# Optimization experiments

Hardware: AMD Instinct MI355X
Metric: run time of the kernel (lower is better)

Reference implementation:

```python
import jax, jax.numpy as jnp
import numpy as np

N, E = 4096, 131072
IN_DIM, HID, H = 128, 64, 8
D = HID * H          # 512 = d_model
DFF = HID * 4        # 256 (source uses hidden_dim*4, not d_model*4)
NEG_SLOPE = 0.2
LN_EPS = 1e-5


def setup_inputs() -> dict:
    key = jax.random.key(0)
    ks = jax.random.split(key, 24)
    r = lambda i, shp, s=0.05: (jax.random.normal(ks[i], shp, jnp.float32) * s)
    return {
        "x": jax.random.normal(ks[0], (N, IN_DIM), jnp.float32),
        "edge_index": jax.random.randint(ks[1], (2, E), 0, N, dtype=jnp.int32),
        "batch": jnp.zeros((N,), jnp.int32),
        "gat_lin_w": r(2, (D, IN_DIM)),
        "gat_att_src": r(3, (H, HID)),
        "gat_att_dst": r(4, (H, HID)),
        "gat_bias": jnp.zeros((D,), jnp.float32),
        "qkv_w": r(5, (2, 3 * D, D)),
        "qkv_b": jnp.zeros((2, 3 * D), jnp.float32),
        "out_w": r(6, (2, D, D)),
        "out_b": jnp.zeros((2, D), jnp.float32),
        "ln1_g": jnp.ones((2, D), jnp.float32),
        "ln1_b": jnp.zeros((2, D), jnp.float32),
        "ff1_w": r(7, (2, DFF, D)),
        "ff1_b": jnp.zeros((2, DFF), jnp.float32),
        "ff2_w": r(8, (2, D, DFF)),
        "ff2_b": jnp.zeros((2, D), jnp.float32),
        "ln2_g": jnp.ones((2, D), jnp.float32),
        "ln2_b": jnp.zeros((2, D), jnp.float32),
    }


def _layer_norm(x, g, b):
    mu = jnp.mean(x, -1, keepdims=True)
    var = jnp.mean(jnp.square(x - mu), -1, keepdims=True)
    return (x - mu) * jax.lax.rsqrt(var + LN_EPS) * g + b


def _gat(x, edge_index, lin_w, att_src, att_dst, bias):
    # PyG GATConv: linear -> per-edge leaky_relu attention -> softmax over dst -> scatter-add
    h = (x @ lin_w.T).reshape(N, H, HID)                 # [N,H,C]
    loops = jnp.arange(N, dtype=edge_index.dtype)        # add_self_loops=True (PyG default)
    src = jnp.concatenate([edge_index[0], loops])
    dst = jnp.concatenate([edge_index[1], loops])
    a_src = jnp.einsum('nhc,hc->nh', h, att_src)         # [N,H]
    a_dst = jnp.einsum('nhc,hc->nh', h, att_dst)
    e = jax.nn.leaky_relu(a_src[src] + a_dst[dst], NEG_SLOPE)   # [E+N,H]
    emax = jax.ops.segment_max(e, dst, num_segments=N)          # self-loops => no empty segment
    p = jnp.exp(e - emax[dst])
    denom = jax.ops.segment_sum(p, dst, num_segments=N)
    alpha = p / (denom[dst] + 1e-16)                             # [E+N,H]
    msg = alpha[..., None] * h[src]                              # [E+N,H,C]
    out = jax.ops.segment_sum(msg, dst, num_segments=N)         # [N,H,C]
    return out.reshape(N, D) + bias


def _mha(x, w_qkv, b_qkv, w_o, b_o):
    qkv = x @ w_qkv.T + b_qkv                            # [N,3D]
    q, k, v = jnp.split(qkv, 3, axis=-1)
    q = q.reshape(N, H, HID).transpose(1, 0, 2)          # [H,N,c]
    k = k.reshape(N, H, HID).transpose(1, 0, 2)
    v = v.reshape(N, H, HID).transpose(1, 0, 2)
    scores = jnp.einsum('hnc,hmc->hnm', q, k) / jnp.sqrt(jnp.float32(HID))
    attn = jax.nn.softmax(scores, axis=-1)
    o = jnp.einsum('hnm,hmc->hnc', attn, v).transpose(1, 0, 2).reshape(N, D)
    return o @ w_o.T + b_o


def reference(x, edge_index, batch, gat_lin_w, gat_att_src, gat_att_dst, gat_bias,
              qkv_w, qkv_b, out_w, out_b, ln1_g, ln1_b,
              ff1_w, ff1_b, ff2_w, ff2_b, ln2_g, ln2_b):
    h = _gat(x, edge_index, gat_lin_w, gat_att_src, gat_att_dst, gat_bias)
    # TransformerEncoder, 2 post-norm layers, relu FFN, dropout=0; seq_len=N, batch=1
    for i in range(2):
        a = _mha(h, qkv_w[i], qkv_b[i], out_w[i], out_b[i])
        h = _layer_norm(h + a, ln1_g[i], ln1_b[i])
        f = jax.nn.relu(h @ ff1_w[i].T + ff1_b[i]) @ ff2_w[i].T + ff2_b[i]
        h = _layer_norm(h + f, ln2_g[i], ln2_b[i])
    return h
```

## Files before the change

kernel.cpp:

```cpp
#include <hip/hip_runtime.h>
#include <math.h>

#define NN    4096
#define EE    131072
#define ENE   (EE + NN)
#define IND   128
#define HH    8
#define HIDC  64
#define DD    512
#define D3    1536
#define DFF2  256

typedef __attribute__((ext_vector_type(8))) short short8;
typedef __attribute__((ext_vector_type(4))) float f32x4;
typedef __attribute__((ext_vector_type(2))) unsigned int uint2v;

__device__ __forceinline__ float lrelu02(float x) { return x >= 0.f ? x : 0.2f * x; }

__device__ __forceinline__ unsigned short f2bf(float x) {
    unsigned int u = __float_as_uint(x);
    u += 0x7fffu + ((u >> 16) & 1u);
    return (unsigned short)(u >> 16);
}
__device__ __forceinline__ float bf2f(unsigned short u) {
    return __uint_as_float((unsigned int)u << 16);
}
__device__ __forceinline__ unsigned int cvt_pk_bf16(float lo, float hi) {
    unsigned int r;
    asm("v_cvt_pk_bf16_f32 %0, %1, %2" : "=v"(r) : "v"(lo), "v"(hi));
    return r;
}
__device__ __forceinline__ float max3f(float a, float b, float c) {
    float r;
    asm("v_max3_f32 %0, %1, %2, %3" : "=v"(r) : "v"(a), "v"(b), "v"(c));
    return r;
}

struct CvtJobs {
    const float* src[6];
    unsigned short* dst[6];
    int n[6];
};

__global__ __launch_bounds__(256) void cvt_many(CvtJobs jb, int total)
{
    int i = (blockIdx.x * 256 + threadIdx.x) * 4;
    if (i >= total) return;
    int s = 0;
    while (i >= jb.n[s]) { i -= jb.n[s]; ++s; }
    float4 v = *(const float4*)(jb.src[s] + i);
    unsigned int lo = (unsigned int)f2bf(v.x) | ((unsigned int)f2bf(v.y) << 16);
    unsigned int hi = (unsigned int)f2bf(v.z) | ((unsigned int)f2bf(v.w) << 16);
    uint2v pk; pk.x = lo; pk.y = hi;
    *(uint2v*)(jb.dst[s] + i) = pk;
}

__global__ __launch_bounds__(256) void gemm_bf16(const unsigned short* __restrict__ A,
                                                 const unsigned short* __restrict__ W,
                                                 const float* __restrict__ bias,
                                                 void* __restrict__ C,
                                                 int M, int K, int N, int flags)
{
    __shared__ __align__(16) unsigned short As[128 * 64];
    __shared__ __align__(16) unsigned short Bs[128 * 64];

    const int t = threadIdx.x, lane = t & 63, w = t >> 6;
    const int wr = w >> 1, wc = w & 1;
    const int bm = blockIdx.y * 128, bn = blockIdx.x * 128;
    const int q = lane & 15, g = lane >> 4;

    f32x4 acc[4][4];
#pragma unroll
    for (int m = 0; m < 4; ++m)
#pragma unroll
        for (int n = 0; n < 4; ++n) acc[m][n] = (f32x4){0.f, 0.f, 0.f, 0.f};

    const int srow = t >> 1, sh = t & 1;
    const unsigned short* Ag = A + (size_t)(bm + srow) * K + sh * 32;
    const unsigned short* Wg = W + (size_t)(bn + srow) * K + sh * 32;
    int wofs[4];
#pragma unroll
    for (int i = 0; i < 4; ++i)
        wofs[i] = srow * 128 + ((((sh * 4 + i) * 16) ^ ((srow & 7) << 4)));

    for (int k0 = 0; k0 < K; k0 += 64) {
        short8 av[4], bv[4];
#pragma unroll
        for (int i = 0; i < 4; ++i) {
            av[i] = *(const short8*)(Ag + k0 + i * 8);
            bv[i] = *(const short8*)(Wg + k0 + i * 8);
        }
        __syncthreads();
#pragma unroll
        for (int i = 0; i < 4; ++i) {
            *(short8*)((char*)As + wofs[i]) = av[i];
            *(short8*)((char*)Bs + wofs[i]) = bv[i];
        }
        __syncthreads();

        short8 af[2][4], bfr[2][4];
#pragma unroll
        for (int m = 0; m < 4; ++m) {
            const int row = wr * 64 + m * 16 + q;
#pragma unroll
            for (int kk = 0; kk < 2; ++kk)
                af[kk][m] = *(const short8*)((const char*)As +
                    row * 128 + ((((kk * 4 + g) * 16) ^ ((row & 7) << 4))));
        }
#pragma unroll
        for (int n = 0; n < 4; ++n) {
            const int row = wc * 64 + n * 16 + q;
#pragma unroll
            for (int kk = 0; kk < 2; ++kk)
                bfr[kk][n] = *(const short8*)((const char*)Bs +
                    row * 128 + ((((kk * 4 + g) * 16) ^ ((row & 7) << 4))));
        }
#pragma unroll
        for (int kk = 0; kk < 2; ++kk)
#pragma unroll
            for (int m = 0; m < 4; ++m)
#pragma unroll
                for (int n = 0; n < 4; ++n)
                    acc[m][n] = __builtin_amdgcn_mfma_f32_16x16x32_bf16(
                        bfr[kk][n], af[kk][m], acc[m][n], 0, 0, 0);
    }

    const int obf = flags & 1, orelu = flags & 2, oqs = flags & 4;
#pragma unroll
    for (int m = 0; m < 4; ++m) {
        const int row = bm + wr * 64 + m * 16 + q;
#pragma unroll
        for (int n = 0; n < 4; ++n) {
            const int col0 = bn + wc * 64 + n * 16 + g * 4;
            f32x4 v = acc[m][n];
            if (bias) {
                float4 bv4 = *(const float4*)(bias + col0);
                v[0] += bv4.x; v[1] += bv4.y; v[2] += bv4.z; v[3] += bv4.w;
            }
            if (oqs && col0 < DD) {
                const float qs = 0.18033688f;
                v[0] *= qs; v[1] *= qs; v[2] *= qs; v[3] *= qs;
            }
            if (orelu) {
                v[0] = fmaxf(v[0], 0.f); v[1] = fmaxf(v[1], 0.f);
                v[2] = fmaxf(v[2], 0.f); v[3] = fmaxf(v[3], 0.f);
            }
            if (obf) {
                uint2v pk;
                pk.x = (unsigned int)f2bf(v[0]) | ((unsigned int)f2bf(v[1]) << 16);
                pk.y = (unsigned int)f2bf(v[2]) | ((unsigned int)f2bf(v[3]) << 16);
                *(uint2v*)((unsigned short*)C + (size_t)row * N + col0) = pk;
            } else {
                float4 o; o.x = v[0]; o.y = v[1]; o.z = v[2]; o.w = v[3];
                *(float4*)((float*)C + (size_t)row * N + col0) = o;
            }
        }
    }
}

__global__ __launch_bounds__(256) void gemm64(const unsigned short* __restrict__ A,
                                              const unsigned short* __restrict__ W,
                                              const float* __restrict__ bias,
                                              void* __restrict__ C,
                                              int M, int K, int N, int flags)
{
    __shared__ __align__(16) unsigned short As[64 * 64];
    __shared__ __align__(16) unsigned short Bs[64 * 64];

    const int t = threadIdx.x, lane = t & 63, w = t >> 6;
    const int wr = w >> 1, wc = w & 1;
    const int bm = blockIdx.y * 64, bn = blockIdx.x * 64;
    const int q = lane & 15, g = lane >> 4;

    f32x4 acc[2][2];
#pragma unroll
    for (int m = 0; m < 2; ++m)
#pragma unroll
        for (int n = 0; n < 2; ++n) acc[m][n] = (f32x4){0.f, 0.f, 0.f, 0.f};

    const int srow = t >> 2, sh = t & 3;
    const unsigned short* Ag = A + (size_t)(bm + srow) * K + sh * 16;
    const unsigned short* Wg = W + (size_t)(bn + srow) * K + sh * 16;
    int wofs[2];
#pragma unroll
    for (int i = 0; i < 2; ++i)
        wofs[i] = srow * 128 + ((((sh * 2 + i) * 16) ^ ((srow & 7) << 4)));

    for (int k0 = 0; k0 < K; k0 += 64) {
        short8 av[2], bv[2];
#pragma unroll
        for (int i = 0; i < 2; ++i) {
            av[i] = *(const short8*)(Ag + k0 + i * 8);
            bv[i] = *(const short8*)(Wg + k0 + i * 8);
        }
        __syncthreads();
#pragma unroll
        for (int i = 0; i < 2; ++i) {
            *(short8*)((char*)As + wofs[i]) = av[i];
            *(short8*)((char*)Bs + wofs[i]) = bv[i];
        }
        __syncthreads();

        short8 af[2][2], bfr[2][2];
#pragma unroll
        for (int m = 0; m < 2; ++m) {
            const int row = wr * 32 + m * 16 + q;
#pragma unroll
            for (int kk = 0; kk < 2; ++kk)
                af[kk][m] = *(const short8*)((const char*)As +
                    row * 128 + ((((kk * 4 + g) * 16) ^ ((row & 7) << 4))));
        }
#pragma unroll
        for (int n = 0; n < 2; ++n) {
            const int row = wc * 32 + n * 16 + q;
#pragma unroll
            for (int kk = 0; kk < 2; ++kk)
                bfr[kk][n] = *(const short8*)((const char*)Bs +
                    row * 128 + ((((kk * 4 + g) * 16) ^ ((row & 7) << 4))));
        }
#pragma unroll
        for (int kk = 0; kk < 2; ++kk)
#pragma unroll
            for (int m = 0; m < 2; ++m)
#pragma unroll
                for (int n = 0; n < 2; ++n)
                    acc[m][n] = __builtin_amdgcn_mfma_f32_16x16x32_bf16(
                        bfr[kk][n], af[kk][m], acc[m][n], 0, 0, 0);
    }

    const int obf = flags & 1, orelu = flags & 2;
#pragma unroll
    for (int m = 0; m < 2; ++m) {
        const int row = bm + wr * 32 + m * 16 + q;
#pragma unroll
        for (int n = 0; n < 2; ++n) {
            const int col0 = bn + wc * 32 + n * 16 + g * 4;
            f32x4 v = acc[m][n];
            if (bias) {
                float4 bv4 = *(const float4*)(bias + col0);
                v[0] += bv4.x; v[1] += bv4.y; v[2] += bv4.z; v[3] += bv4.w;
            }
            if (orelu) {
                v[0] = fmaxf(v[0], 0.f); v[1] = fmaxf(v[1], 0.f);
                v[2] = fmaxf(v[2], 0.f); v[3] = fmaxf(v[3], 0.f);
            }
            if (obf) {
                uint2v pk;
                pk.x = (unsigned int)f2bf(v[0]) | ((unsigned int)f2bf(v[1]) << 16);
                pk.y = (unsigned int)f2bf(v[2]) | ((unsigned int)f2bf(v[3]) << 16);
                *(uint2v*)((unsigned short*)C + (size_t)row * N + col0) = pk;
            } else {
                float4 o; o.x = v[0]; o.y = v[1]; o.z = v[2]; o.w = v[3];
                *(float4*)((float*)C + (size_t)row * N + col0) = o;
            }
        }
    }
}

__global__ void att_proj(const unsigned short* __restrict__ hlin,
                         const float* __restrict__ att_s,
                         const float* __restrict__ att_d,
                         float* __restrict__ a_src, float* __restrict__ a_dst)
{
    int idx = blockIdx.x * 256 + threadIdx.x;
    if (idx >= NN * HH) return;
    int n = idx >> 3, h = idx & 7;
    const unsigned short* hp = hlin + (size_t)n * DD + h * HIDC;
    const float* as = att_s + h * HIDC;
    const float* ad = att_d + h * HIDC;
    float s1 = 0.f, s2 = 0.f;
#pragma unroll 8
    for (int c = 0; c < HIDC; ++c) {
        float hv = bf2f(hp[c]);
        s1 += hv * as[c]; s2 += hv * ad[c];
    }
    a_src[idx] = s1;
    a_dst[idx] = s2;
}

__global__ void hist_kernel(const int* __restrict__ ei, int* __restrict__ counts)
{
    int i = blockIdx.x * 256 + threadIdx.x;
    if (i >= ENE) return;
    int dst = (i < EE) ? ei[EE + i] : (i - EE);
    atomicAdd(&counts[dst], 1);
}

__global__ __launch_bounds__(1024) void scan_kernel(const int* __restrict__ counts,
                                                    int* __restrict__ offsets)
{
    __shared__ int sums[1024];
    int t = threadIdx.x;
    int v0 = counts[t*4+0], v1 = counts[t*4+1], v2 = counts[t*4+2], v3 = counts[t*4+3];
    sums[t] = v0 + v1 + v2 + v3;
    __syncthreads();
    for (int off = 1; off < 1024; off <<= 1) {
        int x = (t >= off) ? sums[t - off] : 0;
        __syncthreads();
        sums[t] += x;
        __syncthreads();
    }
    int pre = (t > 0) ? sums[t-1] : 0;
    offsets[t*4+0] = pre;
    offsets[t*4+1] = pre + v0;
    offsets[t*4+2] = pre + v0 + v1;
    offsets[t*4+3] = pre + v0 + v1 + v2;
    if (t == 1023) offsets[4096] = sums[1023];
}

__global__ void scatter_kernel(const int* __restrict__ ei, const int* __restrict__ offs,
                               int* __restrict__ cursor, int* __restrict__ src_sorted)
{
    int i = blockIdx.x * 256 + threadIdx.x;
    if (i >= ENE) return;
    int s, d;
    if (i < EE) { s = ei[i]; d = ei[EE + i]; } else { s = d = i - EE; }
    int pos = atomicAdd(&cursor[d], 1);
    src_sorted[offs[d] + pos] = s;
}

__global__ __launch_bounds__(256) void gat_node(const unsigned short* __restrict__ hlin,
                                                const float* __restrict__ a_src,
                                                const float* __restrict__ a_dst,
                                                const int* __restrict__ offs,
                                                const int* __restrict__ src_sorted,
                                                const float* __restrict__ bias,
                                                float* __restrict__ out,
                                                unsigned short* __restrict__ outb)
{
    __shared__ float adst[8];
    __shared__ float emax[8];
    __shared__ float denom[8];
    __shared__ float red[256];
    __shared__ float p_lds[16][8];
    __shared__ int   srcs[16];

    const int n = blockIdx.x, t = threadIdx.x;
    if (t < 8) { adst[t] = a_dst[n * 8 + t]; denom[t] = 0.f; }
    const int off0 = offs[n];
    const int deg  = offs[n+1] - off0;
    __syncthreads();

    const int h = t & 7, slot = t >> 3;
    float mx = -3.0e38f;
    for (int j = slot; j < deg; j += 32) {
        int s = src_sorted[off0 + j];
        mx = fmaxf(mx, a_src[s * 8 + h] + adst[h]);
    }
    red[t] = mx;
    __syncthreads();
    for (int half = 128; half >= 8; half >>= 1) {
        if (t < half) red[t] = fmaxf(red[t], red[t + half]);
        __syncthreads();
    }
    if (t < 8) emax[t] = lrelu02(red[t]);
    __syncthreads();

    float acc0 = 0.f, acc1 = 0.f;
    const int h0 = t >> 6, h1 = (t + 256) >> 6;
    for (int base = 0; base < deg; base += 16) {
        int cnt = min(16, deg - base);
        if (t < cnt * 8) {
            int j = base + (t >> 3);
            int s = src_sorted[off0 + j];
            if ((t & 7) == 0) srcs[t >> 3] = s;
            float x = a_src[s * 8 + (t & 7)] + adst[t & 7];
            float p = __expf(lrelu02(x) - emax[t & 7]);
            p_lds[t >> 3][t & 7] = p;
            atomicAdd(&denom[t & 7], p);
        }
        __syncthreads();
        for (int jj = 0; jj < cnt; ++jj) {
            int s = srcs[jj];
            const unsigned short* hp = hlin + (size_t)s * DD;
            acc0 += p_lds[jj][h0] * bf2f(hp[t]);
            acc1 += p_lds[jj][h1] * bf2f(hp[256 + t]);
        }
        __syncthreads();
    }
    float o0 = acc0 / (denom[h0] + 1e-16f) + bias[t];
    float o1 = acc1 / (denom[h1] + 1e-16f) + bias[256 + t];
    out[(size_t)n * DD + t]        = o0;
    out[(size_t)n * DD + 256 + t]  = o1;
    outb[(size_t)n * DD + t]       = f2bf(o0);
    outb[(size_t)n * DD + 256 + t] = f2bf(o1);
}

#define KVB 128
#define NTT (NN / KVB)

__global__ __launch_bounds__(256) void attn_mfma(const unsigned short* __restrict__ qkv,
                                                 unsigned short* __restrict__ aob)
{
    __shared__ __align__(16) unsigned short Ks0[KVB * 64];
    __shared__ __align__(16) unsigned short Vt0[80 * KVB];
    __shared__ __align__(16) unsigned short Ks1[KVB * 64];
    __shared__ __align__(16) unsigned short Vt1[80 * KVB];

    const int t = threadIdx.x;
    const int w = t >> 6, lane = t & 63;
    const int q15 = lane & 15, g = lane >> 4;

    const int fid = blockIdx.x;
    const int h = fid & 7, qb = fid >> 3;
    const int qbase = qb * 64 + w * 16;

    const unsigned short* qrow = qkv + (size_t)(qbase + q15) * D3 + h * HIDC;
    const short8 qf0 = *(const short8*)(qrow + g * 8);
    const short8 qf1 = *(const short8*)(qrow + 32 + g * 8);

    f32x4 O[4];
#pragma unroll
    for (int db = 0; db < 4; ++db) O[db] = (f32x4){0.f, 0.f, 0.f, 0.f};
    f32x4 O5 = (f32x4){0.f, 0.f, 0.f, 0.f};
    float m_run = -3.0e38f;

    int koff[8][2];
#pragma unroll
    for (int kvb = 0; kvb < 8; ++kvb) {
        const int kr = kvb * 16 + q15;
        koff[kvb][0] = (kr * 64 + g * 8) ^ ((kr & 7) << 3);
        koff[kvb][1] = (kr * 64 + 32 + g * 8) ^ ((kr & 7) << 3);
    }
    int voff[4][4];
#pragma unroll
    for (int db = 0; db < 4; ++db) {
        const int vr = db * 16 + q15;
#pragma unroll
        for (int ks = 0; ks < 4; ++ks)
            voff[db][ks] = (vr * KVB + ks * 32 + g * 8) ^ ((vr & 7) << 3);
    }
    int voffE[4];
#pragma unroll
    for (int ks = 0; ks < 4; ++ks) {
        const int rv = 64 + q15;
        voffE[ks] = (rv * KVB + ks * 32 + g * 8) ^ ((rv & 7) << 3);
    }
    const int kr_s = t >> 1, sh = t & 1;
    const int kq = t & 31, dg = t >> 5;
    const int slot4 = (kq >> 3) * 32 + (kq & 3) * 8 + ((kq >> 2) & 1) * 4;
    int kwoff[4];
#pragma unroll
    for (int i = 0; i < 4; ++i)
        kwoff[i] = (kr_s * 64 + (sh * 4 + i) * 8) ^ ((kr_s & 7) << 3);
    int vwoff[8];
#pragma unroll
    for (int i = 0; i < 8; ++i) {
        const int d = dg * 8 + i;
        vwoff[i] = (d * KVB + slot4) ^ ((d & 7) << 3);
    }
    const unsigned short* Kg = qkv + (size_t)kr_s * D3 + DD + h * HIDC + sh * 32;
    const unsigned short* Vg = qkv + (size_t)(4 * kq) * D3 + 2 * DD + h * HIDC + dg * 8;

    short8 kreg[4], vreg[4];

    auto LOAD_KV = [&](int kb) {
        const size_t off = (size_t)kb * KVB * D3;
#pragma unroll
        for (int i = 0; i < 4; ++i) kreg[i] = *(const short8*)(Kg + off + i * 8);
#pragma unroll
        for (int jj = 0; jj < 4; ++jj) vreg[jj] = *(const short8*)(Vg + off + (size_t)jj * D3);
    };
    auto WRITE_KV = [&](unsigned short* KD, unsigned short* VD) {
#pragma unroll
        for (int i = 0; i < 4; ++i)
            *(short8*)&KD[kwoff[i]] = kreg[i];
        const unsigned int* w0 = (const unsigned int*)&vreg[0];
        const unsigned int* w1 = (const unsigned int*)&vreg[1];
        const unsigned int* w2 = (const unsigned int*)&vreg[2];
        const unsigned int* w3 = (const unsigned int*)&vreg[3];
#pragma unroll
        for (int i = 0; i < 8; ++i) {
            const unsigned int sel = (i & 1) ? 0x07060302u : 0x05040100u;
            uint2v pk;
            pk.x = __builtin_amdgcn_perm(w1[i >> 1], w0[i >> 1], sel);
            pk.y = __builtin_amdgcn_perm(w3[i >> 1], w2[i >> 1], sel);
            *(uint2v*)&VD[vwoff[i]] = pk;
        }
    };

    auto TILE = [&](int kb, const unsigned short* BK, const unsigned short* BV,
                    unsigned short* NK, unsigned short* NV) {
        const int kbn = kb + 1;
        if (kbn < NTT) LOAD_KV(kbn);

        f32x4 st[8];
        __builtin_amdgcn_s_setprio(1);
#pragma unroll
        for (int kvb = 0; kvb < 8; ++kvb) {
            const short8 kf0 = *(const short8*)&BK[koff[kvb][0]];
            const short8 kf1 = *(const short8*)&BK[koff[kvb][1]];
            f32x4 acc = (f32x4){0.f, 0.f, 0.f, 0.f};
            acc = __builtin_amdgcn_mfma_f32_16x16x32_bf16(kf0, qf0, acc, 0, 0, 0);
            acc = __builtin_amdgcn_mfma_f32_16x16x32_bf16(kf1, qf1, acc, 0, 0, 0);
            st[kvb] = acc;
        }
        __builtin_amdgcn_s_setprio(0);

        float pm0 = max3f(st[0][0], st[0][1], st[0][2]);
        float pm1 = max3f(st[0][3], st[1][0], st[1][1]);
        float pm2 = max3f(st[1][2], st[1][3], st[2][0]);
        float pm3 = max3f(st[2][1], st[2][2], st[2][3]);
        float pm4 = max3f(st[3][0], st[3][1], st[3][2]);
        float pm5 = max3f(st[3][3], st[4][0], st[4][1]);
        float pm6 = max3f(st[4][2], st[4][3], st[5][0]);
        float pm7 = max3f(st[5][1], st[5][2], st[5][3]);
        float pm8 = max3f(st[6][0], st[6][1], st[6][2]);
        float pm9 = max3f(st[6][3], st[7][0], st[7][1]);
        float pmA = max3f(st[7][2], st[7][3], pm0);
        float q0 = max3f(pm1, pm2, pm3);
        float q1 = max3f(pm4, pm5, pm6);
        float q2 = max3f(pm7, pm8, pm9);
        float pmax = max3f(q0, q1, q2);
        pmax = fmaxf(pmax, pmA);
        pmax = fmaxf(pmax, __shfl_xor(pmax, 16, 64));
        pmax = fmaxf(pmax, __shfl_xor(pmax, 32, 64));
        if (!__all(pmax <= m_run + 11.f)) {
            const float mnew = fmaxf(m_run, pmax);
            const float f = exp2f(m_run - mnew);
#pragma unroll
            for (int db = 0; db < 4; ++db) O[db] *= f;
            O5 *= f;
            m_run = mnew;
        }

        short8 pf[4];
#pragma unroll
        for (int ks = 0; ks < 4; ++ks) {
            float e0 = exp2f(st[2*ks  ][0] - m_run), e1 = exp2f(st[2*ks  ][1] - m_run);
            float e2 = exp2f(st[2*ks  ][2] - m_run), e3 = exp2f(st[2*ks  ][3] - m_run);
            float e4 = exp2f(st[2*ks+1][0] - m_run), e5 = exp2f(st[2*ks+1][1] - m_run);
            float e6 = exp2f(st[2*ks+1][2] - m_run), e7 = exp2f(st[2*ks+1][3] - m_run);
            union { unsigned int u[4]; short8 s8; } pu;
            pu.u[0] = cvt_pk_bf16(e0, e1);
            pu.u[1] = cvt_pk_bf16(e2, e3);
            pu.u[2] = cvt_pk_bf16(e4, e5);
            pu.u[3] = cvt_pk_bf16(e6, e7);
            pf[ks] = pu.s8;
        }

        __builtin_amdgcn_s_setprio(1);
#pragma unroll
        for (int db = 0; db < 4; ++db) {
#pragma unroll
            for (int ks = 0; ks < 4; ++ks) {
                const short8 vf = *(const short8*)&BV[voff[db][ks]];
                O[db] = __builtin_amdgcn_mfma_f32_16x16x32_bf16(vf, pf[ks], O[db], 0, 0, 0);
            }
        }
#pragma unroll
        for (int ks = 0; ks < 4; ++ks) {
            const short8 vfE = *(const short8*)&BV[voffE[ks]];
            O5 = __builtin_amdgcn_mfma_f32_16x16x32_bf16(vfE, pf[ks], O5, 0, 0, 0);
        }
        __builtin_amdgcn_s_setprio(0);

        if (kbn < NTT) {
            WRITE_KV(NK, NV);
            __syncthreads();
        }
    };

    {
        const int d = 64 + (t >> 4), c = (t & 15) * 8;
        short8 iv;
#pragma unroll
        for (int i = 0; i < 8; ++i)
            iv[i] = (short)((d == 64) ? 0x3F80 : 0);
        const int ofs = (d * KVB + c) ^ ((d & 7) << 3);
        *(short8*)&Vt0[ofs] = iv;
        *(short8*)&Vt1[ofs] = iv;
    }
    LOAD_KV(0);
    WRITE_KV(Ks0, Vt0);
    __syncthreads();

    for (int kb = 0; kb < NTT; kb += 2) {
        TILE(kb,     Ks0, Vt0, Ks1, Vt1);
        TILE(kb + 1, Ks1, Vt1, Ks0, Vt0);
    }

    const float lsum = __shfl(O5[0], q15, 64);
    const float linv = 1.f / lsum;
#pragma unroll
    for (int db = 0; db < 4; ++db) {
        uint2v pk;
        pk.x = (unsigned int)f2bf(O[db][0] * linv) | ((unsigned int)f2bf(O[db][1] * linv) << 16);
        pk.y = (unsigned int)f2bf(O[db][2] * linv) | ((unsigned int)f2bf(O[db][3] * linv) << 16);
        *(uint2v*)&aob[(size_t)(qbase + q15) * DD + h * HIDC + db * 16 + g * 4] = pk;
    }
}

__global__ __launch_bounds__(256) void ln_fused(const float* __restrict__ hin,
                                                const float* __restrict__ dlt,
                                                const float* __restrict__ g,
                                                const float* __restrict__ b,
                                                float* __restrict__ out,
                                                unsigned short* __restrict__ outb)
{
    __shared__ float red[256];
    const int r = blockIdx.x, t = threadIdx.x;
    const size_t base = (size_t)r * DD;
    float v0 = hin[base + t] + dlt[base + t];
    float v1 = hin[base + 256 + t] + dlt[base + 256 + t];
    red[t] = v0 + v1;
    __syncthreads();
    for (int off = 128; off > 0; off >>= 1) { if (t < off) red[t] += red[t + off]; __syncthreads(); }
    float mu = red[0] * (1.f / 512.f);
    __syncthreads();
    float d0 = v0 - mu, d1 = v1 - mu;
    red[t] = d0 * d0 + d1 * d1;
    __syncthreads();
    for (int off = 128; off > 0; off >>= 1) { if (t < off) red[t] += red[t + off]; __syncthreads(); }
    float rs = rsqrtf(red[0] * (1.f / 512.f) + 1e-5f);
    float o0 = d0 * rs * g[t] + b[t];
    float o1 = d1 * rs * g[256 + t] + b[256 + t];
    out[base + t]       = o0;
    out[base + 256 + t] = o1;
    if (outb) {
        outb[base + t]       = f2bf(o0);
        outb[base + 256 + t] = f2bf(o1);
    }
}

extern "C" void kernel_launch(void* const* d_in, const int* in_sizes, int n_in,
                              void* d_out, int out_size, void* d_ws, size_t ws_size,
                              hipStream_t stream)
{
    (void)in_sizes; (void)n_in; (void)out_size; (void)ws_size;

    const float* x        = (const float*)d_in[0];
    const int*   ei       = (const int*)  d_in[1];
    const float* lin_w    = (const float*)d_in[3];
    const float* att_src  = (const float*)d_in[4];
    const float* att_dst  = (const float*)d_in[5];
    const float* gat_bias = (const float*)d_in[6];
    const float* qkv_w    = (const float*)d_in[7];
    const float* qkv_b    = (const float*)d_in[8];
    const float* out_w    = (const float*)d_in[9];
    const float* out_b    = (const float*)d_in[10];
    const float* ln1_g    = (const float*)d_in[11];
    const float* ln1_b    = (const float*)d_in[12];
    const float* ff1_w    = (const float*)d_in[13];
    const float* ff1_b    = (const float*)d_in[14];
    const float* ff2_w    = (const float*)d_in[15];
    const float* ff2_b    = (const float*)d_in[16];
    const float* ln2_g    = (const float*)d_in[17];
    const float* ln2_b    = (const float*)d_in[18];

    char* wsb = (char*)d_ws;
    size_t o = 0;
    auto alloc = [&](size_t bytes) { char* p = wsb + o; o += (bytes + 255) & ~(size_t)255; return p; };

    unsigned short* hlin_bf = (unsigned short*)alloc((size_t)NN * DD * 2);
    unsigned short* hbf     = (unsigned short*)alloc((size_t)NN * DD * 2);
    unsigned short* qkv16   = (unsigned short*)alloc((size_t)NN * D3 * 2);
    unsigned short* aob     = (unsigned short*)alloc((size_t)NN * DD * 2);
    unsigned short* ff1obf  = (unsigned short*)alloc((size_t)NN * DFF2 * 2);
    float* hcur  = (float*)alloc((size_t)NN * DD * 4);
    float* tmp1  = (float*)alloc((size_t)NN * DD * 4);
    float* a_src = (float*)alloc((size_t)NN * HH * 4);
    float* a_dst = (float*)alloc((size_t)NN * HH * 4);
    int* counts     = (int*)alloc(NN * 4);
    int* cursor     = (int*)alloc(NN * 4);
    int* offsets    = (int*)alloc((NN + 1) * 4);
    int* src_sorted = (int*)alloc(ENE * 4);
    unsigned short* xbf    = (unsigned short*)alloc((size_t)NN * IND * 2);
    unsigned short* linwbf = (unsigned short*)alloc((size_t)DD * IND * 2);
    unsigned short* qkvwbf = (unsigned short*)alloc((size_t)2 * D3 * DD * 2);
    unsigned short* outwbf = (unsigned short*)alloc((size_t)2 * DD * DD * 2);
    unsigned short* ff1wbf = (unsigned short*)alloc((size_t)2 * DFF2 * DD * 2);
    unsigned short* ff2wbf = (unsigned short*)alloc((size_t)2 * DD * DFF2 * 2);

    CvtJobs jb;
    jb.src[0] = x;      jb.dst[0] = xbf;    jb.n[0] = NN * IND;
    jb.src[1] = lin_w;  jb.dst[1] = linwbf; jb.n[1] = DD * IND;
    jb.src[2] = qkv_w;  jb.dst[2] = qkvwbf; jb.n[2] = 2 * D3 * DD;
    jb.src[3] = out_w;  jb.dst[3] = outwbf; jb.n[3] = 2 * DD * DD;
    jb.src[4] = ff1_w;  jb.dst[4] = ff1wbf; jb.n[4] = 2 * DFF2 * DD;
    jb.src[5] = ff2_w;  jb.dst[5] = ff2wbf; jb.n[5] = 2 * DD * DFF2;
    int cvt_total = jb.n[0]+jb.n[1]+jb.n[2]+jb.n[3]+jb.n[4]+jb.n[5];
    cvt_many<<<(cvt_total/4 + 255)/256, 256, 0, stream>>>(jb, cvt_total);

    hipMemsetAsync(counts, 0, 2 * NN * sizeof(int), stream);
    gemm64<<<dim3(DD/64, NN/64), 256, 0, stream>>>(xbf, linwbf, nullptr, hlin_bf,
                                                   NN, IND, DD, 1);
    att_proj<<<(NN*HH + 255)/256, 256, 0, stream>>>(hlin_bf, att_src, att_dst, a_src, a_dst);
    hist_kernel<<<(ENE + 255)/256, 256, 0, stream>>>(ei, counts);
    scan_kernel<<<1, 1024, 0, stream>>>(counts, offsets);
    scatter_kernel<<<(ENE + 255)/256, 256, 0, stream>>>(ei, offsets, cursor, src_sorted);
    gat_node<<<NN, 256, 0, stream>>>(hlin_bf, a_src, a_dst, offsets, src_sorted, gat_bias,
                                     hcur, hbf);

    for (int i = 0; i < 2; ++i) {
        gemm_bf16<<<dim3(D3/128, NN/128), 256, 0, stream>>>(hbf, qkvwbf + (size_t)i*D3*DD,
                                                            qkv_b + (size_t)i*D3, qkv16,
                                                            NN, DD, D3, 1 | 4);
        attn_mfma<<<dim3(NN/64 * HH), 256, 0, stream>>>(qkv16, aob);
        gemm64<<<dim3(DD/64, NN/64), 256, 0, stream>>>(aob, outwbf + (size_t)i*DD*DD,
                                                       out_b + (size_t)i*DD, tmp1,
                                                       NN, DD, DD, 0);
        ln_fused<<<NN, 256, 0, stream>>>(hcur, tmp1, ln1_g + (size_t)i*DD, ln1_b + (size_t)i*DD,
                                         hcur, hbf);
        gemm64<<<dim3(DFF2/64, NN/64), 256, 0, stream>>>(hbf, ff1wbf + (size_t)i*DFF2*DD,
                                                         ff1_b + (size_t)i*DFF2, ff1obf,
                                                         NN, DD, DFF2, 1 | 2);
        gemm64<<<dim3(DD/64, NN/64), 256, 0, stream>>>(ff1obf, ff2wbf + (size_t)i*DD*DFF2,
                                                       ff2_b + (size_t)i*DD, tmp1,
                                                       NN, DFF2, DD, 0);
        float* outp = (i == 1) ? (float*)d_out : hcur;
        unsigned short* outbp = (i == 1) ? nullptr : hbf;
        ln_fused<<<NN, 256, 0, stream>>>(hcur, tmp1, ln2_g + (size_t)i*DD, ln2_b + (size_t)i*DD,
                                         outp, outbp);
    }
}
```

Baseline: 332.8 us.

## Process two query tiles per wave in attention, store residual deltas as bf16

```diff
diff --git a/kernel.cpp b/kernel.cpp
--- a/kernel.cpp
+++ b/kernel.cpp
@@ -389,8 +389,8 @@
 #define KVB 128
 #define NTT (NN / KVB)
 
-__global__ __launch_bounds__(256) void attn_mfma(const unsigned short* __restrict__ qkv,
-                                                 unsigned short* __restrict__ aob)
+__global__ __launch_bounds__(128, 1) void attn_mfma(const unsigned short* __restrict__ qkv,
+                                                    unsigned short* __restrict__ aob)
 {
     __shared__ __align__(16) unsigned short Ks0[KVB * 64];
     __shared__ __align__(16) unsigned short Vt0[80 * KVB];
@@ -403,17 +403,24 @@
 
     const int fid = blockIdx.x;
     const int h = fid & 7, qb = fid >> 3;
-    const int qbase = qb * 64 + w * 16;
-
-    const unsigned short* qrow = qkv + (size_t)(qbase + q15) * D3 + h * HIDC;
-    const short8 qf0 = *(const short8*)(qrow + g * 8);
-    const short8 qf1 = *(const short8*)(qrow + 32 + g * 8);
-
-    f32x4 O[4];
-#pragma unroll
-    for (int db = 0; db < 4; ++db) O[db] = (f32x4){0.f, 0.f, 0.f, 0.f};
-    f32x4 O5 = (f32x4){0.f, 0.f, 0.f, 0.f};
-    float m_run = -3.0e38f;
+    const int qbase = qb * 64 + w * 32;
+
+    const unsigned short* qrow0 = qkv + (size_t)(qbase + q15) * D3 + h * HIDC;
+    const unsigned short* qrow1 = qrow0 + (size_t)16 * D3;
+    const short8 qf00 = *(const short8*)(qrow0 + g * 8);
+    const short8 qf01 = *(const short8*)(qrow0 + 32 + g * 8);
+    const short8 qf10 = *(const short8*)(qrow1 + g * 8);
+    const short8 qf11 = *(const short8*)(qrow1 + 32 + g * 8);
+
+    f32x4 O0[4], O1[4];
+#pragma unroll
+    for (int db = 0; db < 4; ++db) {
+        O0[db] = (f32x4){0.f, 0.f, 0.f, 0.f};
+        O1[db] = (f32x4){0.f, 0.f, 0.f, 0.f};
+    }
+    f32x4 O5a = (f32x4){0.f, 0.f, 0.f, 0.f};
+    f32x4 O5b = (f32x4){0.f, 0.f, 0.f, 0.f};
+    float m0 = -3.0e38f, m1 = -3.0e38f;
 
     int koff[8][2];
 #pragma unroll
@@ -436,46 +443,53 @@
         const int rv = 64 + q15;
         voffE[ks] = (rv * KVB + ks * 32 + g * 8) ^ ((rv & 7) << 3);
     }
-    const int kr_s = t >> 1, sh = t & 1;
+
+    const int krow = t;
     const int kq = t & 31, dg = t >> 5;
     const int slot4 = (kq >> 3) * 32 + (kq & 3) * 8 + ((kq >> 2) & 1) * 4;
-    int kwoff[4];
-#pragma unroll
-    for (int i = 0; i < 4; ++i)
-        kwoff[i] = (kr_s * 64 + (sh * 4 + i) * 8) ^ ((kr_s & 7) << 3);
-    int vwoff[8];
-#pragma unroll
-    for (int i = 0; i < 8; ++i) {
-        const int d = dg * 8 + i;
+    int kwoff[8];
+#pragma unroll
+    for (int i = 0; i < 8; ++i)
+        kwoff[i] = (krow * 64 + i * 8) ^ ((krow & 7) << 3);
+    int vwoff[16];
+#pragma unroll
+    for (int i = 0; i < 16; ++i) {
+        const int d = dg * 16 + i;
         vwoff[i] = (d * KVB + slot4) ^ ((d & 7) << 3);
     }
-    const unsigned short* Kg = qkv + (size_t)kr_s * D3 + DD + h * HIDC + sh * 32;
-    const unsigned short* Vg = qkv + (size_t)(4 * kq) * D3 + 2 * DD + h * HIDC + dg * 8;
-
-    short8 kreg[4], vreg[4];
+    const unsigned short* Kg = qkv + (size_t)krow * D3 + DD + h * HIDC;
+    const unsigned short* Vg = qkv + (size_t)(4 * kq) * D3 + 2 * DD + h * HIDC + dg * 16;
+
+    short8 kreg[8], vreg[4][2];
 
     auto LOAD_KV = [&](int kb) {
         const size_t off = (size_t)kb * KVB * D3;
 #pragma unroll
-        for (int i = 0; i < 4; ++i) kreg[i] = *(const short8*)(Kg + off + i * 8);
-#pragma unroll
-        for (int jj = 0; jj < 4; ++jj) vreg[jj] = *(const short8*)(Vg + off + (size_t)jj * D3);
+        for (int i = 0; i < 8; ++i) kreg[i] = *(const short8*)(Kg + off + i * 8);
+#pragma unroll
+        for (int j = 0; j < 4; ++j)
+#pragma unroll
+            for (int c = 0; c < 2; ++c)
+                vreg[j][c] = *(const short8*)(Vg + off + (size_t)j * D3 + c * 8);
     };
     auto WRITE_KV = [&](unsigned short* KD, unsigned short* VD) {
 #pragma unroll
-        for (int i = 0; i < 4; ++i)
+        for (int i = 0; i < 8; ++i)
             *(short8*)&KD[kwoff[i]] = kreg[i];
-        const unsigned int* w0 = (const unsigned int*)&vreg[0];
-        const unsigned int* w1 = (const unsigned int*)&vreg[1];
-        const unsigned int* w2 = (const unsigned int*)&vreg[2];
-        const unsigned int* w3 = (const unsigned int*)&vreg[3];
-#pragma unroll
-        for (int i = 0; i < 8; ++i) {
-            const unsigned int sel = (i & 1) ? 0x07060302u : 0x05040100u;
-            uint2v pk;
-            pk.x = __builtin_amdgcn_perm(w1[i >> 1], w0[i >> 1], sel);
-            pk.y = __builtin_amdgcn_perm(w3[i >> 1], w2[i >> 1], sel);
-            *(uint2v*)&VD[vwoff[i]] = pk;
+#pragma unroll
+        for (int c = 0; c < 2; ++c) {
+            const unsigned int* w0 = (const unsigned int*)&vreg[0][c];
+            const unsigned int* w1 = (const unsigned int*)&vreg[1][c];
+            const unsigned int* w2 = (const unsigned int*)&vreg[2][c];
+            const unsigned int* w3 = (const unsigned int*)&vreg[3][c];
+#pragma unroll
+            for (int i = 0; i < 8; ++i) {
+                const unsigned int sel = (i & 1) ? 0x07060302u : 0x05040100u;
+                uint2v pk;
+                pk.x = __builtin_amdgcn_perm(w1[i >> 1], w0[i >> 1], sel);
+                pk.y = __builtin_amdgcn_perm(w3[i >> 1], w2[i >> 1], sel);
+                *(uint2v*)&VD[vwoff[c * 8 + i]] = pk;
+            }
         }
     };
 
@@ -484,59 +498,71 @@
         const int kbn = kb + 1;
         if (kbn < NTT) LOAD_KV(kbn);
 
-        f32x4 st[8];
+        f32x4 st0[8], st1[8];
         __builtin_amdgcn_s_setprio(1);
 #pragma unroll
         for (int kvb = 0; kvb < 8; ++kvb) {
             const short8 kf0 = *(const short8*)&BK[koff[kvb][0]];
             const short8 kf1 = *(const short8*)&BK[koff[kvb][1]];
-            f32x4 acc = (f32x4){0.f, 0.f, 0.f, 0.f};
-            acc = __builtin_amdgcn_mfma_f32_16x16x32_bf16(kf0, qf0, acc, 0, 0, 0);
-            acc = __builtin_amdgcn_mfma_f32_16x16x32_bf16(kf1, qf1, acc, 0, 0, 0);
-            st[kvb] = acc;
+            f32x4 a0 = (f32x4){0.f, 0.f, 0.f, 0.f};
+            f32x4 a1 = (f32x4){0.f, 0.f, 0.f, 0.f};
+            a0 = __builtin_amdgcn_mfma_f32_16x16x32_bf16(kf0, qf00, a0, 0, 0, 0);
+            a1 = __builtin_amdgcn_mfma_f32_16x16x32_bf16(kf0, qf10, a1, 0, 0, 0);
+            a0 = __builtin_amdgcn_mfma_f32_16x16x32_bf16(kf1, qf01, a0, 0, 0, 0);
+            a1 = __builtin_amdgcn_mfma_f32_16x16x32_bf16(kf1, qf11, a1, 0, 0, 0);
+            st0[kvb] = a0;
+            st1[kvb] = a1;
         }
         __builtin_amdgcn_s_setprio(0);
 
-        float pm0 = max3f(st[0][0], st[0][1], st[0][2]);
-        float pm1 = max3f(st[0][3], st[1][0], st[1][1]);
-        float pm2 = max3f(st[1][2], st[1][3], st[2][0]);
-        float pm3 = max3f(st[2][1], st[2][2], st[2][3]);
-        float pm4 = max3f(st[3][0], st[3][1], st[3][2]);
-        float pm5 = max3f(st[3][3], st[4][0], st[4][1]);
-        float pm6 = max3f(st[4][2], st[4][3], st[5][0]);
-        float pm7 = max3f(st[5][1], st[5][2], st[5][3]);
-        float pm8 = max3f(st[6][0], st[6][1], st[6][2]);
-        float pm9 = max3f(st[6][3], st[7][0], st[7][1]);
-        float pmA = max3f(st[7][2], st[7][3], pm0);
-        float q0 = max3f(pm1, pm2, pm3);
-        float q1 = max3f(pm4, pm5, pm6);
-        float q2 = max3f(pm7, pm8, pm9);
-        float pmax = max3f(q0, q1, q2);
-        pmax = fmaxf(pmax, pmA);
-        pmax = fmaxf(pmax, __shfl_xor(pmax, 16, 64));
-        pmax = fmaxf(pmax, __shfl_xor(pmax, 32, 64));
-        if (!__all(pmax <= m_run + 11.f)) {
-            const float mnew = fmaxf(m_run, pmax);
-            const float f = exp2f(m_run - mnew);
-#pragma unroll
-            for (int db = 0; db < 4; ++db) O[db] *= f;
-            O5 *= f;
-            m_run = mnew;
-        }
-
-        short8 pf[4];
-#pragma unroll
-        for (int ks = 0; ks < 4; ++ks) {
-            float e0 = exp2f(st[2*ks  ][0] - m_run), e1 = exp2f(st[2*ks  ][1] - m_run);
-            float e2 = exp2f(st[2*ks  ][2] - m_run), e3 = exp2f(st[2*ks  ][3] - m_run);
-            float e4 = exp2f(st[2*ks+1][0] - m_run), e5 = exp2f(st[2*ks+1][1] - m_run);
-            float e6 = exp2f(st[2*ks+1][2] - m_run), e7 = exp2f(st[2*ks+1][3] - m_run);
-            union { unsigned int u[4]; short8 s8; } pu;
-            pu.u[0] = cvt_pk_bf16(e0, e1);
-            pu.u[1] = cvt_pk_bf16(e2, e3);
-            pu.u[2] = cvt_pk_bf16(e4, e5);
-            pu.u[3] = cvt_pk_bf16(e6, e7);
-            pf[ks] = pu.s8;
+        short8 pf0[4], pf1[4];
+#pragma unroll
+        for (int qg = 0; qg < 2; ++qg) {
+            f32x4* st = qg ? st1 : st0;
+            f32x4* O  = qg ? O1  : O0;
+            f32x4& O5 = qg ? O5b : O5a;
+            float& m_run = qg ? m1 : m0;
+            short8* pf = qg ? pf1 : pf0;
+
+            float pm0 = max3f(st[0][0], st[0][1], st[0][2]);
+            float pm1 = max3f(st[0][3], st[1][0], st[1][1]);
+            float pm2 = max3f(st[1][2], st[1][3], st[2][0]);
+            float pm3 = max3f(st[2][1], st[2][2], st[2][3]);
+            float pm4 = max3f(st[3][0], st[3][1], st[3][2]);
+            float pm5 = max3f(st[3][3], st[4][0], st[4][1]);
+            float pm6 = max3f(st[4][2], st[4][3], st[5][0]);
+            float pm7 = max3f(st[5][1], st[5][2], st[5][3]);
+            float pm8 = max3f(st[6][0], st[6][1], st[6][2]);
+            float pm9 = max3f(st[6][3], st[7][0], st[7][1]);
+            float pmA = max3f(st[7][2], st[7][3], pm0);
+            float r0 = max3f(pm1, pm2, pm3);
+            float r1 = max3f(pm4, pm5, pm6);
+            float r2 = max3f(pm7, pm8, pm9);
+            float pmax = max3f(r0, r1, r2);
+            pmax = fmaxf(pmax, pmA);
+            pmax = fmaxf(pmax, __shfl_xor(pmax, 16, 64));
+            pmax = fmaxf(pmax, __shfl_xor(pmax, 32, 64));
+            if (!__all(pmax <= m_run + 11.f)) {
+                const float mnew = fmaxf(m_run, pmax);
+                const float f = exp2f(m_run - mnew);
+#pragma unroll
+                for (int db = 0; db < 4; ++db) O[db] *= f;
+                O5 *= f;
+                m_run = mnew;
+            }
+#pragma unroll
+            for (int ks = 0; ks < 4; ++ks) {
+                float e0 = exp2f(st[2*ks  ][0] - m_run), e1 = exp2f(st[2*ks  ][1] - m_run);
+                float e2 = exp2f(st[2*ks  ][2] - m_run), e3 = exp2f(st[2*ks  ][3] - m_run);
+                float e4 = exp2f(st[2*ks+1][0] - m_run), e5 = exp2f(st[2*ks+1][1] - m_run);
+                float e6 = exp2f(st[2*ks+1][2] - m_run), e7 = exp2f(st[2*ks+1][3] - m_run);
+                union { unsigned int u[4]; short8 s8; } pu;
+                pu.u[0] = cvt_pk_bf16(e0, e1);
+                pu.u[1] = cvt_pk_bf16(e2, e3);
+                pu.u[2] = cvt_pk_bf16(e4, e5);
+                pu.u[3] = cvt_pk_bf16(e6, e7);
+                pf[ks] = pu.s8;
+            }
         }
 
         __builtin_amdgcn_s_setprio(1);
@@ -545,13 +571,15 @@
 #pragma unroll
             for (int ks = 0; ks < 4; ++ks) {
                 const short8 vf = *(const short8*)&BV[voff[db][ks]];
-                O[db] = __builtin_amdgcn_mfma_f32_16x16x32_bf16(vf, pf[ks], O[db], 0, 0, 0);
+                O0[db] = __builtin_amdgcn_mfma_f32_16x16x32_bf16(vf, pf0[ks], O0[db], 0, 0, 0);
+                O1[db] = __builtin_amdgcn_mfma_f32_16x16x32_bf16(vf, pf1[ks], O1[db], 0, 0, 0);
             }
         }
 #pragma unroll
         for (int ks = 0; ks < 4; ++ks) {
             const short8 vfE = *(const short8*)&BV[voffE[ks]];
-            O5 = __builtin_amdgcn_mfma_f32_16x16x32_bf16(vfE, pf[ks], O5, 0, 0, 0);
+            O5a = __builtin_amdgcn_mfma_f32_16x16x32_bf16(vfE, pf0[ks], O5a, 0, 0, 0);
+            O5b = __builtin_amdgcn_mfma_f32_16x16x32_bf16(vfE, pf1[ks], O5b, 0, 0, 0);
         }
         __builtin_amdgcn_s_setprio(0);
 
@@ -562,14 +590,15 @@
     };
 
     {
-        const int d = 64 + (t >> 4), c = (t & 15) * 8;
+        const int d = 64 + (t >> 3), c = (t & 7) * 16;
         short8 iv;
 #pragma unroll
         for (int i = 0; i < 8; ++i)
             iv[i] = (short)((d == 64) ? 0x3F80 : 0);
-        const int ofs = (d * KVB + c) ^ ((d & 7) << 3);
-        *(short8*)&Vt0[ofs] = iv;
-        *(short8*)&Vt1[ofs] = iv;
+        const int ofs0 = (d * KVB + c) ^ ((d & 7) << 3);
+        const int ofs1 = (d * KVB + c + 8) ^ ((d & 7) << 3);
+        *(short8*)&Vt0[ofs0] = iv; *(short8*)&Vt0[ofs1] = iv;
+        *(short8*)&Vt1[ofs0] = iv; *(short8*)&Vt1[ofs1] = iv;
     }
     LOAD_KV(0);
     WRITE_KV(Ks0, Vt0);
@@ -580,19 +609,25 @@
         TILE(kb + 1, Ks1, Vt1, Ks0, Vt0);
     }
 
-    const float lsum = __shfl(O5[0], q15, 64);
-    const float linv = 1.f / lsum;
-#pragma unroll
-    for (int db = 0; db < 4; ++db) {
-        uint2v pk;
-        pk.x = (unsigned int)f2bf(O[db][0] * linv) | ((unsigned int)f2bf(O[db][1] * linv) << 16);
-        pk.y = (unsigned int)f2bf(O[db][2] * linv) | ((unsigned int)f2bf(O[db][3] * linv) << 16);
-        *(uint2v*)&aob[(size_t)(qbase + q15) * DD + h * HIDC + db * 16 + g * 4] = pk;
+#pragma unroll
+    for (int qg = 0; qg < 2; ++qg) {
+        const f32x4* O  = qg ? O1  : O0;
+        const f32x4& O5 = qg ? O5b : O5a;
+        const float lsum = __shfl(O5[0], q15, 64);
+        const float linv = 1.f / lsum;
+        const size_t row = (size_t)(qbase + qg * 16 + q15);
+#pragma unroll
+        for (int db = 0; db < 4; ++db) {
+            uint2v pk;
+            pk.x = (unsigned int)f2bf(O[db][0] * linv) | ((unsigned int)f2bf(O[db][1] * linv) << 16);
+            pk.y = (unsigned int)f2bf(O[db][2] * linv) | ((unsigned int)f2bf(O[db][3] * linv) << 16);
+            *(uint2v*)&aob[row * DD + h * HIDC + db * 16 + g * 4] = pk;
+        }
     }
 }
 
 __global__ __launch_bounds__(256) void ln_fused(const float* __restrict__ hin,
-                                                const float* __restrict__ dlt,
+                                                const unsigned short* __restrict__ dlt,
                                                 const float* __restrict__ g,
                                                 const float* __restrict__ b,
                                                 float* __restrict__ out,
@@ -601,8 +636,10 @@
     __shared__ float red[256];
     const int r = blockIdx.x, t = threadIdx.x;
     const size_t base = (size_t)r * DD;
-    float v0 = hin[base + t] + dlt[base + t];
-    float v1 = hin[base + 256 + t] + dlt[base + 256 + t];
+    float2 hv = *(const float2*)(hin + base + 2 * t);
+    unsigned int dv = *(const unsigned int*)(dlt + base + 2 * t);
+    float v0 = hv.x + bf2f((unsigned short)(dv & 0xffffu));
+    float v1 = hv.y + bf2f((unsigned short)(dv >> 16));
     red[t] = v0 + v1;
     __syncthreads();
     for (int off = 128; off > 0; off >>= 1) { if (t < off) red[t] += red[t + off]; __syncthreads(); }
@@ -613,13 +650,15 @@
     __syncthreads();
     for (int off = 128; off > 0; off >>= 1) { if (t < off) red[t] += red[t + off]; __syncthreads(); }
     float rs = rsqrtf(red[0] * (1.f / 512.f) + 1e-5f);
-    float o0 = d0 * rs * g[t] + b[t];
-    float o1 = d1 * rs * g[256 + t] + b[256 + t];
-    out[base + t]       = o0;
-    out[base + 256 + t] = o1;
+    float2 gv = *(const float2*)(g + 2 * t);
+    float2 bv = *(const float2*)(b + 2 * t);
+    float o0 = d0 * rs * gv.x + bv.x;
+    float o1 = d1 * rs * gv.y + bv.y;
+    float2 ov; ov.x = o0; ov.y = o1;
+    *(float2*)(out + base + 2 * t) = ov;
     if (outb) {
-        outb[base + t]       = f2bf(o0);
-        outb[base + 256 + t] = f2bf(o1);
+        unsigned int pk = (unsigned int)f2bf(o0) | ((unsigned int)f2bf(o1) << 16);
+        *(unsigned int*)(outb + base + 2 * t) = pk;
     }
 }
 
@@ -657,8 +696,8 @@
     unsigned short* qkv16   = (unsigned short*)alloc((size_t)NN * D3 * 2);
     unsigned short* aob     = (unsigned short*)alloc((size_t)NN * DD * 2);
     unsigned short* ff1obf  = (unsigned short*)alloc((size_t)NN * DFF2 * 2);
+    unsigned short* dltbf   = (unsigned short*)alloc((size_t)NN * DD * 2);
     float* hcur  = (float*)alloc((size_t)NN * DD * 4);
-    float* tmp1  = (float*)alloc((size_t)NN * DD * 4);
     float* a_src = (float*)alloc((size_t)NN * HH * 4);
     float* a_dst = (float*)alloc((size_t)NN * HH * 4);
     int* counts     = (int*)alloc(NN * 4);
@@ -696,21 +735,21 @@
         gemm_bf16<<<dim3(D3/128, NN/128), 256, 0, stream>>>(hbf, qkvwbf + (size_t)i*D3*DD,
                                                             qkv_b + (size_t)i*D3, qkv16,
                                                             NN, DD, D3, 1 | 4);
-        attn_mfma<<<dim3(NN/64 * HH), 256, 0, stream>>>(qkv16, aob);
+        attn_mfma<<<dim3(NN/64 * HH), 128, 0, stream>>>(qkv16, aob);
         gemm64<<<dim3(DD/64, NN/64), 256, 0, stream>>>(aob, outwbf + (size_t)i*DD*DD,
-                                                       out_b + (size_t)i*DD, tmp1,
-                                                       NN, DD, DD, 0);
-        ln_fused<<<NN, 256, 0, stream>>>(hcur, tmp1, ln1_g + (size_t)i*DD, ln1_b + (size_t)i*DD,
+                                                       out_b + (size_t)i*DD, dltbf,
+                                                       NN, DD, DD, 1);
+        ln_fused<<<NN, 256, 0, stream>>>(hcur, dltbf, ln1_g + (size_t)i*DD, ln1_b + (size_t)i*DD,
                                          hcur, hbf);
         gemm64<<<dim3(DFF2/64, NN/64), 256, 0, stream>>>(hbf, ff1wbf + (size_t)i*DFF2*DD,
                                                          ff1_b + (size_t)i*DFF2, ff1obf,
                                                          NN, DD, DFF2, 1 | 2);
         gemm64<<<dim3(DD/64, NN/64), 256, 0, stream>>>(ff1obf, ff2wbf + (size_t)i*DD*DFF2,
-                                                       ff2_b + (size_t)i*DD, tmp1,
-                                                       NN, DFF2, DD, 0);
+                                                       ff2_b + (size_t)i*DD, dltbf,
+                                                       NN, DFF2, DD, 1);
         float* outp = (i == 1) ? (float*)d_out : hcur;
         unsigned short* outbp = (i == 1) ? nullptr : hbf;
-        ln_fused<<<NN, 256, 0, stream>>>(hcur, tmp1, ln2_g + (size_t)i*DD, ln2_b + (size_t)i*DD,
+        ln_fused<<<NN, 256, 0, stream>>>(hcur, dltbf, ln2_g + (size_t)i*DD, ln2_b + (size_t)i*DD,
                                          outp, outbp);
     }
 }
```

New measurement: 448.9 us. 34.9% more time.
